# Performance work log

Measured on AMD Instinct MI355X. Metric: run time of the kernel, lower is better.

Reference implementation:

```python
import jax, jax.numpy as jnp
import numpy as np

KERNEL_MUL = 2.0
KERNEL_NUM = 5


def _mmd(source, target):
    n = source.shape[0]
    m = target.shape[0]
    total = jnp.concatenate([source, target], axis=0)  # [n+m, d]
    sq = jnp.sum(total * total, axis=1)  # [n+m]
    l2 = sq[:, None] + sq[None, :] - 2.0 * (total @ total.T)  # [n+m, n+m]
    l2 = jnp.maximum(l2, 0.0)
    n_samples = n + m
    bandwidth = jnp.sum(l2) / (n_samples * n_samples - n_samples)
    bandwidth = bandwidth / (KERNEL_MUL ** (KERNEL_NUM // 2))
    # sum of KERNEL_NUM Gaussian kernels with geometric bandwidths
    kernels = sum(jnp.exp(-l2 / (bandwidth * KERNEL_MUL ** i)) for i in range(KERNEL_NUM))
    b = n  # batch_size = n, as in the torch code
    xx = jnp.sum(kernels[:b, :b]) / (n * n)
    yy = jnp.sum(kernels[b:, b:]) / (m * m)
    xy = jnp.sum(kernels[:b, b:]) / (n * m)
    yx = jnp.sum(kernels[b:, :b]) / (m * n)
    return xx + yy - xy - yx


def setup_inputs() -> dict:
    key = jax.random.key(0)
    k1, k2 = jax.random.split(key)
    source = jax.random.normal(k1, (4096, 256), dtype=jnp.float32)
    target = jax.random.normal(k2, (4096, 256), dtype=jnp.float32)
    return {"source": source, "target": target}


def reference(source, target):
    return _mmd(source, target)
```

## Files before the change

### kernel.cpp

```cpp
#include <hip/hip_runtime.h>
#include <hip/hip_bf16.h>

#define WS_SLOT_OFF   0
#define WS_NEGG_OFF   16640
#define WS_SQPART_OFF 16648
#define WS_CSPART_OFF 17672
#define WS_SQ_OFF     148744
#define WS_G_OFF      181520

#define NROW 8192
#define HALF 4096
#define DIM  256
#define TILE 128
#define NB   64
#define NBLK (NB * (NB + 1) / 2)
#define KC   32
#define NC   (DIM / KC)
#define BUFE (TILE * KC)
#define PREPB 128

typedef short  short8 __attribute__((ext_vector_type(8)));
typedef float  f32x4  __attribute__((ext_vector_type(4)));
typedef float  f32x2  __attribute__((ext_vector_type(2)));
typedef unsigned short us4 __attribute__((ext_vector_type(4)));

static __device__ __forceinline__ unsigned short f2bfbits(float f) {
    __hip_bfloat16 h = __float2bfloat16(f);
    return *reinterpret_cast<unsigned short*>(&h);
}
static __device__ __forceinline__ float bfbits2f(unsigned short u) {
    return __uint_as_float(((unsigned int)u) << 16);
}
static __device__ __forceinline__ void gl_lds16(const void* g, void* l) {
    __builtin_amdgcn_global_load_lds(
        (const __attribute__((address_space(1))) void*)g,
        (__attribute__((address_space(3))) void*)l, 16, 0, 0);
}

__global__ __launch_bounds__(256) void k_prep(const float* __restrict__ src,
                                              const float* __restrict__ tgt,
                                              unsigned short* __restrict__ G,
                                              float* __restrict__ sq,
                                              float* __restrict__ cspart,
                                              double* __restrict__ sqpart) {
    __shared__ float cs_lds[4 * 256];
    __shared__ double sq_lds[4];

    int t = threadIdx.x, wid = t >> 6, lane = t & 63;
    int r0 = blockIdx.x * 64;
    int c4 = lane * 4;

    float cs0 = 0.f, cs1 = 0.f, cs2 = 0.f, cs3 = 0.f;
    double wsq = 0.0;
    for (int i = 0; i < 16; ++i) {
        int row = r0 + wid + i * 4;
        const float* base = (row < HALF) ? (src + (size_t)row * DIM)
                                         : (tgt + (size_t)(row - HALF) * DIM);
        float4 v = *(const float4*)(base + c4);
        unsigned short u0 = f2bfbits(v.x), u1 = f2bfbits(v.y),
                       u2 = f2bfbits(v.z), u3 = f2bfbits(v.w);
        us4 uu = {u0, u1, u2, u3};
        *(us4*)(G + (size_t)row * DIM + c4) = uu;
        float r0f = bfbits2f(u0), r1f = bfbits2f(u1),
              r2f = bfbits2f(u2), r3f = bfbits2f(u3);
        cs0 += r0f; cs1 += r1f; cs2 += r2f; cs3 += r3f;
        float s = r0f * r0f + r1f * r1f + r2f * r2f + r3f * r3f;
        #pragma unroll
        for (int off = 32; off; off >>= 1) s += __shfl_down(s, off);
        if (lane == 0) { sq[row] = s; wsq += (double)s; }
    }
    cs_lds[wid * 256 + c4 + 0] = cs0;
    cs_lds[wid * 256 + c4 + 1] = cs1;
    cs_lds[wid * 256 + c4 + 2] = cs2;
    cs_lds[wid * 256 + c4 + 3] = cs3;
    if (lane == 0) sq_lds[wid] = wsq;
    __syncthreads();
    float s = cs_lds[t] + cs_lds[256 + t] + cs_lds[512 + t] + cs_lds[768 + t];
    cspart[blockIdx.x * 256 + t] = s;
    if (t == 0)
        sqpart[blockIdx.x] = sq_lds[0] + sq_lds[1] + sq_lds[2] + sq_lds[3];
}

__global__ __launch_bounds__(256) void k_bw(const float* __restrict__ cspart,
                                            const double* __restrict__ sqpart,
                                            double* __restrict__ negg) {
    __shared__ double red[256];
    __shared__ double red2[256];
    int t = threadIdx.x;
    double c = 0.0;
    for (int b = 0; b < PREPB; ++b) c += (double)cspart[b * 256 + t];
    double s = (t < PREPB) ? sqpart[t] : 0.0;
    red[t]  = s;
    red2[t] = c * c;
    __syncthreads();
    for (int off = 128; off; off >>= 1) {
        if (t < off) { red[t] += red[t + off]; red2[t] += red2[t + off]; }
        __syncthreads();
    }
    if (t == 0) {
        const double N = (double)NROW;
        double sum_l2 = 2.0 * N * red[0] - 2.0 * red2[0];
        double bw = sum_l2 / (N * N - N);
        bw = bw / 4.0;
        negg[0] = -1.4426950408889634 / (16.0 * bw);
    }
}

__global__ __launch_bounds__(256, 3) void k_mmd(const unsigned short* __restrict__ G,
                                                const float* __restrict__ sq,
                                                const double* __restrict__ negg,
                                                double* __restrict__ slots) {
    __shared__ unsigned short As[2 * BUFE];
    __shared__ unsigned short Bs[2 * BUFE];
    __shared__ double wsum[4];

    int bi = 0, rem = blockIdx.x;
    while (rem >= NB - bi) { rem -= NB - bi; ++bi; }
    int bj = bi + rem;

    int t = threadIdx.x, wid = t >> 6, lane = t & 63;
    int wr = wid >> 1, wc = wid & 1;
    int rl = lane & 15, klane = lane >> 4;

    const unsigned short* Abase = G + (size_t)bi * TILE * DIM;
    const unsigned short* Bbase = G + (size_t)bj * TILE * DIM;

    int lr0 = wid * 32 + (lane >> 2);
    int slog0 = (lane & 3) ^ ((lr0 >> 1) & 3);
    int lr1 = lr0 + 16;
    int slog1 = (lane & 3) ^ ((lr1 >> 1) & 3);
    size_t ga0 = (size_t)lr0 * DIM + slog0 * 8;
    size_t ga1 = (size_t)lr1 * DIM + slog1 * 8;
    int ld0 = (wid * 32) * KC;
    int ld1 = (wid * 32 + 16) * KC;

    int aoff[4], boff[4];
    #pragma unroll
    for (int f = 0; f < 4; ++f) {
        int ra = wr * 64 + f * 16 + rl;
        aoff[f] = ra * KC + ((klane ^ ((ra >> 1) & 3)) * 8);
        int rb = wc * 64 + f * 16 + rl;
        boff[f] = rb * KC + ((klane ^ ((rb >> 1) & 3)) * 8);
    }

    const f32x4 zero4 = {0.f, 0.f, 0.f, 0.f};
    f32x4 acc[4][4];
    #pragma unroll
    for (int i = 0; i < 4; ++i)
        #pragma unroll
        for (int j = 0; j < 4; ++j) acc[i][j] = zero4;

    #define STAGE(kc, b)                                                     \
        do {                                                                 \
            gl_lds16(Abase + ga0 + (kc) * KC, &As[(b) * BUFE + ld0]);        \
            gl_lds16(Bbase + ga0 + (kc) * KC, &Bs[(b) * BUFE + ld0]);        \
            gl_lds16(Abase + ga1 + (kc) * KC, &As[(b) * BUFE + ld1]);        \
            gl_lds16(Bbase + ga1 + (kc) * KC, &Bs[(b) * BUFE + ld1]);        \
        } while (0)

    STAGE(0, 0);
    #pragma unroll
    for (int kc = 0; kc < NC; ++kc) {
        asm volatile("s_waitcnt vmcnt(0)" ::: "memory");
        __builtin_amdgcn_s_barrier();
        __builtin_amdgcn_sched_barrier(0);
        if (kc + 1 < NC) STAGE(kc + 1, (kc + 1) & 1);

        const unsigned short* Ab = &As[(kc & 1) * BUFE];
        const unsigned short* Bb = &Bs[(kc & 1) * BUFE];
        short8 af[4], bfv[4];
        #pragma unroll
        for (int f = 0; f < 4; ++f) {
            af[f]  = *(const short8*)&Ab[aoff[f]];
            bfv[f] = *(const short8*)&Bb[boff[f]];
        }
        #pragma unroll
        for (int i = 0; i < 4; ++i)
            #pragma unroll
            for (int j = 0; j < 4; ++j)
                acc[i][j] = __builtin_amdgcn_mfma_f32_16x16x32_bf16(
                    af[i], bfv[j], acc[i][j], 0, 0, 0);
    }
    #undef STAGE

    int gi0 = bi * TILE + wr * 64;
    int gj0 = bj * TILE + wc * 64;
    float ng2 = (float)negg[0];
    float m2g = -2.0f * ng2;
    f32x2 m2g2 = {m2g, m2g};
    int rgrp = lane >> 4;

    float sqb4[4];
    #pragma unroll
    for (int j = 0; j < 4; ++j) sqb4[j] = sq[gj0 + j * 16 + rl] * ng2;

    f32x2 tsv = {0.f, 0.f};
    #pragma unroll
    for (int i = 0; i < 4; ++i) {
        int base = gi0 + i * 16 + rgrp * 4;
        f32x2 sa01 = {sq[base + 0] * ng2, sq[base + 1] * ng2};
        f32x2 sa23 = {sq[base + 2] * ng2, sq[base + 3] * ng2};
        #pragma unroll
        for (int j = 0; j < 4; ++j) {
            f32x2 sb = {sqb4[j], sqb4[j]};
            f32x2 x01 = {acc[i][j][0], acc[i][j][1]};
            f32x2 x23 = {acc[i][j][2], acc[i][j][3]};
            x01 = x01 * m2g2 + (sa01 + sb);
            x23 = x23 * m2g2 + (sa23 + sb);
            f32x2 e01, e23;
            e01.x = exp2f(x01.x); e01.y = exp2f(x01.y);
            e23.x = exp2f(x23.x); e23.y = exp2f(x23.y);
            f32x2 p01 = e01 * e01, q01 = p01 * p01,
                  r01 = q01 * q01, s01 = r01 * r01;
            f32x2 p23 = e23 * e23, q23 = p23 * p23,
                  r23 = q23 * q23, s23 = r23 * r23;
            tsv += ((e01 + p01) + (q01 + r01)) + s01;
            tsv += ((e23 + p23) + (q23 + r23)) + s23;
        }
    }
    float tsum = tsv.x + tsv.y;

    float w = ((bi < 32) == (bj < 32)) ? 1.f : -1.f;
    if (bi != bj) w *= 2.f;
    double dsum = (double)tsum * (double)w;

    #pragma unroll
    for (int off = 32; off; off >>= 1) dsum += __shfl_down(dsum, off);
    if (lane == 0) wsum[wid] = dsum;
    __syncthreads();
    if (t == 0)
        slots[blockIdx.x] = wsum[0] + wsum[1] + wsum[2] + wsum[3];
}

__global__ __launch_bounds__(256) void k_final(const double* __restrict__ slots,
                                               float* __restrict__ out) {
    __shared__ double red[256];
    int t = threadIdx.x;
    double s = 0.0;
    for (int i = t; i < NBLK; i += 256) s += slots[i];
    red[t] = s;
    __syncthreads();
    for (int off = 128; off; off >>= 1) {
        if (t < off) red[t] += red[t + off];
        __syncthreads();
    }
    if (t == 0)
        out[0] = (float)(red[0] / ((double)HALF * (double)HALF));
}

extern "C" void kernel_launch(void* const* d_in, const int* in_sizes, int n_in,
                              void* d_out, int out_size, void* d_ws, size_t ws_size,
                              hipStream_t stream) {
    const float* src = (const float*)d_in[0];
    const float* tgt = (const float*)d_in[1];
    float* out = (float*)d_out;

    double* slots     = (double*)((char*)d_ws + WS_SLOT_OFF);
    double* negg      = (double*)((char*)d_ws + WS_NEGG_OFF);
    double* sqpart    = (double*)((char*)d_ws + WS_SQPART_OFF);
    float*  cspart    = (float*)((char*)d_ws + WS_CSPART_OFF);
    float*  sq        = (float*)((char*)d_ws + WS_SQ_OFF);
    unsigned short* G = (unsigned short*)((char*)d_ws + WS_G_OFF);

    k_prep<<<PREPB, 256, 0, stream>>>(src, tgt, G, sq, cspart, sqpart);
    k_bw<<<1, 256, 0, stream>>>(cspart, sqpart, negg);
    k_mmd<<<NBLK, 256, 0, stream>>>(G, sq, negg, slots);
    k_final<<<1, 256, 0, stream>>>(slots, out);
}
```

Measured before the change: 65.65 us.

## Shrink MMD tiles to 64x64 with 32x32x16 MFMA and interleaved block order

Measured after the change: 83.12 us. 1.27x slower.

```diff
diff --git a/kernel.cpp b/kernel.cpp
--- a/kernel.cpp
+++ b/kernel.cpp
@@ -2,26 +2,25 @@
 #include <hip/hip_bf16.h>
 
 #define WS_SLOT_OFF   0
-#define WS_NEGG_OFF   16640
-#define WS_SQPART_OFF 16648
-#define WS_CSPART_OFF 17672
-#define WS_SQ_OFF     148744
-#define WS_G_OFF      181520
+#define WS_NEGG_OFF   66048
+#define WS_SQPART_OFF 66056
+#define WS_CSPART_OFF 67080
+#define WS_SQ_OFF     198152
+#define WS_G_OFF      230928
 
 #define NROW 8192
 #define HALF 4096
 #define DIM  256
-#define TILE 128
-#define NB   64
-#define NBLK (NB * (NB + 1) / 2)
+#define TT   64
+#define NT   128
+#define NPAIR (NT * (NT + 1) / 2)
 #define KC   32
 #define NC   (DIM / KC)
-#define BUFE (TILE * KC)
+#define BUFE (TT * KC)
 #define PREPB 128
 
 typedef short  short8 __attribute__((ext_vector_type(8)));
-typedef float  f32x4  __attribute__((ext_vector_type(4)));
-typedef float  f32x2  __attribute__((ext_vector_type(2)));
+typedef float  f32x16 __attribute__((ext_vector_type(16)));
 typedef unsigned short us4 __attribute__((ext_vector_type(4)));
 
 static __device__ __forceinline__ unsigned short f2bfbits(float f) {
@@ -106,7 +105,7 @@
     }
 }
 
-__global__ __launch_bounds__(256, 3) void k_mmd(const unsigned short* __restrict__ G,
+__global__ __launch_bounds__(256, 6) void k_mmd(const unsigned short* __restrict__ G,
                                                 const float* __restrict__ sq,
                                                 const double* __restrict__ negg,
                                                 double* __restrict__ slots) {
@@ -114,48 +113,39 @@
     __shared__ unsigned short Bs[2 * BUFE];
     __shared__ double wsum[4];
 
-    int bi = 0, rem = blockIdx.x;
-    while (rem >= NB - bi) { rem -= NB - bi; ++bi; }
-    int bj = bi + rem;
+    int bid = blockIdx.x;
+    int p = (bid & 7) * (NPAIR / 8) + (bid >> 3);
+
+    int ti = 0, rem = p;
+    while (rem >= NT - ti) { rem -= NT - ti; ++ti; }
+    int tj = ti + rem;
 
     int t = threadIdx.x, wid = t >> 6, lane = t & 63;
     int wr = wid >> 1, wc = wid & 1;
-    int rl = lane & 15, klane = lane >> 4;
-
-    const unsigned short* Abase = G + (size_t)bi * TILE * DIM;
-    const unsigned short* Bbase = G + (size_t)bj * TILE * DIM;
-
-    int lr0 = wid * 32 + (lane >> 2);
-    int slog0 = (lane & 3) ^ ((lr0 >> 1) & 3);
-    int lr1 = lr0 + 16;
-    int slog1 = (lane & 3) ^ ((lr1 >> 1) & 3);
-    size_t ga0 = (size_t)lr0 * DIM + slog0 * 8;
-    size_t ga1 = (size_t)lr1 * DIM + slog1 * 8;
-    int ld0 = (wid * 32) * KC;
-    int ld1 = (wid * 32 + 16) * KC;
-
-    int aoff[4], boff[4];
-    #pragma unroll
-    for (int f = 0; f < 4; ++f) {
-        int ra = wr * 64 + f * 16 + rl;
-        aoff[f] = ra * KC + ((klane ^ ((ra >> 1) & 3)) * 8);
-        int rb = wc * 64 + f * 16 + rl;
-        boff[f] = rb * KC + ((klane ^ ((rb >> 1) & 3)) * 8);
-    }
-
-    const f32x4 zero4 = {0.f, 0.f, 0.f, 0.f};
-    f32x4 acc[4][4];
-    #pragma unroll
-    for (int i = 0; i < 4; ++i)
-        #pragma unroll
-        for (int j = 0; j < 4; ++j) acc[i][j] = zero4;
-
-    #define STAGE(kc, b)                                                     \
-        do {                                                                 \
-            gl_lds16(Abase + ga0 + (kc) * KC, &As[(b) * BUFE + ld0]);        \
-            gl_lds16(Bbase + ga0 + (kc) * KC, &Bs[(b) * BUFE + ld0]);        \
-            gl_lds16(Abase + ga1 + (kc) * KC, &As[(b) * BUFE + ld1]);        \
-            gl_lds16(Bbase + ga1 + (kc) * KC, &Bs[(b) * BUFE + ld1]);        \
+
+    const unsigned short* Abase = G + (size_t)ti * TT * DIM;
+    const unsigned short* Bbase = G + (size_t)tj * TT * DIM;
+
+    int sslot = (lane & 3) ^ ((lane >> 3) & 3);
+    size_t gsrc = (size_t)(wid * 16 + (lane >> 2)) * DIM + sslot * 8;
+    int ldst = (wid * 16) * KC;
+
+    int ra = wr * 32 + (lane & 31);
+    int rb = wc * 32 + (lane & 31);
+    int sA = lane >> 5;
+    int swa = (ra >> 1) & 3, swb = (rb >> 1) & 3;
+    int aoff0 = ra * KC + ((sA ^ swa) * 8);
+    int aoff1 = ra * KC + (((2 + sA) ^ swa) * 8);
+    int boff0 = rb * KC + ((sA ^ swb) * 8);
+    int boff1 = rb * KC + (((2 + sA) ^ swb) * 8);
+
+    f32x16 acc = {0.f, 0.f, 0.f, 0.f, 0.f, 0.f, 0.f, 0.f,
+                  0.f, 0.f, 0.f, 0.f, 0.f, 0.f, 0.f, 0.f};
+
+    #define STAGE(kc, b)                                                   \
+        do {                                                               \
+            gl_lds16(Abase + gsrc + (kc) * KC, &As[(b) * BUFE + ldst]);    \
+            gl_lds16(Bbase + gsrc + (kc) * KC, &Bs[(b) * BUFE + ldst]);    \
         } while (0)
 
     STAGE(0, 0);
@@ -168,68 +158,45 @@
 
         const unsigned short* Ab = &As[(kc & 1) * BUFE];
         const unsigned short* Bb = &Bs[(kc & 1) * BUFE];
-        short8 af[4], bfv[4];
-        #pragma unroll
-        for (int f = 0; f < 4; ++f) {
-            af[f]  = *(const short8*)&Ab[aoff[f]];
-            bfv[f] = *(const short8*)&Bb[boff[f]];
-        }
-        #pragma unroll
-        for (int i = 0; i < 4; ++i)
-            #pragma unroll
-            for (int j = 0; j < 4; ++j)
-                acc[i][j] = __builtin_amdgcn_mfma_f32_16x16x32_bf16(
-                    af[i], bfv[j], acc[i][j], 0, 0, 0);
+        short8 a0 = *(const short8*)&Ab[aoff0];
+        short8 b0 = *(const short8*)&Bb[boff0];
+        short8 a1 = *(const short8*)&Ab[aoff1];
+        short8 b1 = *(const short8*)&Bb[boff1];
+        acc = __builtin_amdgcn_mfma_f32_32x32x16_bf16(a0, b0, acc, 0, 0, 0);
+        acc = __builtin_amdgcn_mfma_f32_32x32x16_bf16(a1, b1, acc, 0, 0, 0);
     }
     #undef STAGE
 
-    int gi0 = bi * TILE + wr * 64;
-    int gj0 = bj * TILE + wc * 64;
+    int gi0 = ti * TT + wr * 32 + 4 * (lane >> 5);
+    int gj  = tj * TT + wc * 32 + (lane & 31);
     float ng2 = (float)negg[0];
     float m2g = -2.0f * ng2;
-    f32x2 m2g2 = {m2g, m2g};
-    int rgrp = lane >> 4;
-
-    float sqb4[4];
+    float sqb = sq[gj] * ng2;
+
+    float tsum = 0.f;
     #pragma unroll
-    for (int j = 0; j < 4; ++j) sqb4[j] = sq[gj0 + j * 16 + rl] * ng2;
-
-    f32x2 tsv = {0.f, 0.f};
-    #pragma unroll
-    for (int i = 0; i < 4; ++i) {
-        int base = gi0 + i * 16 + rgrp * 4;
-        f32x2 sa01 = {sq[base + 0] * ng2, sq[base + 1] * ng2};
-        f32x2 sa23 = {sq[base + 2] * ng2, sq[base + 3] * ng2};
-        #pragma unroll
-        for (int j = 0; j < 4; ++j) {
-            f32x2 sb = {sqb4[j], sqb4[j]};
-            f32x2 x01 = {acc[i][j][0], acc[i][j][1]};
-            f32x2 x23 = {acc[i][j][2], acc[i][j][3]};
-            x01 = x01 * m2g2 + (sa01 + sb);
-            x23 = x23 * m2g2 + (sa23 + sb);
-            f32x2 e01, e23;
-            e01.x = exp2f(x01.x); e01.y = exp2f(x01.y);
-            e23.x = exp2f(x23.x); e23.y = exp2f(x23.y);
-            f32x2 p01 = e01 * e01, q01 = p01 * p01,
-                  r01 = q01 * q01, s01 = r01 * r01;
-            f32x2 p23 = e23 * e23, q23 = p23 * p23,
-                  r23 = q23 * q23, s23 = r23 * r23;
-            tsv += ((e01 + p01) + (q01 + r01)) + s01;
-            tsv += ((e23 + p23) + (q23 + r23)) + s23;
-        }
-    }
-    float tsum = tsv.x + tsv.y;
-
-    float w = ((bi < 32) == (bj < 32)) ? 1.f : -1.f;
-    if (bi != bj) w *= 2.f;
-    double dsum = (double)tsum * (double)w;
+    for (int q = 0; q < 16; ++q) {
+        int row = (q & 3) + 8 * (q >> 2);
+        float sqa = sq[gi0 + row] * ng2;
+        float x   = fmaf(acc[q], m2g, sqa + sqb);
+        float e   = exp2f(x);
+        float e2  = e * e;
+        float e4  = e2 * e2;
+        float e8  = e4 * e4;
+        float e16 = e8 * e8;
+        tsum += (e + e2) + (e4 + e8) + e16;
+    }
+
+    float w = ((ti < NT / 2) == (tj < NT / 2)) ? 1.f : -1.f;
+    if (ti != tj) w *= 2.f;
+    double dsum = (double)(tsum * w);
 
     #pragma unroll
     for (int off = 32; off; off >>= 1) dsum += __shfl_down(dsum, off);
     if (lane == 0) wsum[wid] = dsum;
     __syncthreads();
     if (t == 0)
-        slots[blockIdx.x] = wsum[0] + wsum[1] + wsum[2] + wsum[3];
+        slots[bid] = wsum[0] + wsum[1] + wsum[2] + wsum[3];
 }
 
 __global__ __launch_bounds__(256) void k_final(const double* __restrict__ slots,
@@ -237,7 +204,7 @@
     __shared__ double red[256];
     int t = threadIdx.x;
     double s = 0.0;
-    for (int i = t; i < NBLK; i += 256) s += slots[i];
+    for (int i = t; i < NPAIR; i += 256) s += slots[i];
     red[t] = s;
     __syncthreads();
     for (int off = 128; off; off >>= 1) {
@@ -264,6 +231,6 @@
 
     k_prep<<<PREPB, 256, 0, stream>>>(src, tgt, G, sq, cspart, sqpart);
     k_bw<<<1, 256, 0, stream>>>(cspart, sqpart, negg);
-    k_mmd<<<NBLK, 256, 0, stream>>>(G, sq, negg, slots);
+    k_mmd<<<NPAIR, 256, 0, stream>>>(G, sq, negg, slots);
     k_final<<<1, 256, 0, stream>>>(slots, out);
 }
```

## Use 256x256 tiles with 512-thread blocks each processing three tile pairs

Applied to the files above, without the earlier changes.

Measured after the change: 70.16 us. +6.9%, slower.

```diff
diff --git a/kernel.cpp b/kernel.cpp
--- a/kernel.cpp
+++ b/kernel.cpp
@@ -2,22 +2,23 @@
 #include <hip/hip_bf16.h>
 
 #define WS_SLOT_OFF   0
-#define WS_NEGG_OFF   16640
-#define WS_SQPART_OFF 16648
-#define WS_CSPART_OFF 17672
-#define WS_SQ_OFF     148744
-#define WS_G_OFF      181520
+#define WS_NEGG_OFF   1408
+#define WS_SQPART_OFF 1416
+#define WS_CSPART_OFF 3464
+#define WS_SQ_OFF     265608
+#define WS_G_OFF      298384
 
 #define NROW 8192
 #define HALF 4096
 #define DIM  256
-#define TILE 128
-#define NB   64
-#define NBLK (NB * (NB + 1) / 2)
+#define TS   256
+#define NTT  32
+#define NP   (NTT * (NTT + 1) / 2)
+#define GRID_MMD (NP / 3)
 #define KC   32
 #define NC   (DIM / KC)
-#define BUFE (TILE * KC)
-#define PREPB 128
+#define ABUF (TS * KC)
+#define PREPB 256
 
 typedef short  short8 __attribute__((ext_vector_type(8)));
 typedef float  f32x4  __attribute__((ext_vector_type(4)));
@@ -47,12 +48,12 @@
     __shared__ double sq_lds[4];
 
     int t = threadIdx.x, wid = t >> 6, lane = t & 63;
-    int r0 = blockIdx.x * 64;
+    int r0 = blockIdx.x * 32;
     int c4 = lane * 4;
 
     float cs0 = 0.f, cs1 = 0.f, cs2 = 0.f, cs3 = 0.f;
     double wsq = 0.0;
-    for (int i = 0; i < 16; ++i) {
+    for (int i = 0; i < 8; ++i) {
         int row = r0 + wid + i * 4;
         const float* base = (row < HALF) ? (src + (size_t)row * DIM)
                                          : (tgt + (size_t)(row - HALF) * DIM);
@@ -89,7 +90,7 @@
     int t = threadIdx.x;
     double c = 0.0;
     for (int b = 0; b < PREPB; ++b) c += (double)cspart[b * 256 + t];
-    double s = (t < PREPB) ? sqpart[t] : 0.0;
+    double s = sqpart[t];
     red[t]  = s;
     red2[t] = c * c;
     __syncthreads();
@@ -106,139 +107,148 @@
     }
 }
 
-__global__ __launch_bounds__(256, 3) void k_mmd(const unsigned short* __restrict__ G,
+__global__ __launch_bounds__(512, 2) void k_mmd(const unsigned short* __restrict__ G,
                                                 const float* __restrict__ sq,
                                                 const double* __restrict__ negg,
                                                 double* __restrict__ slots) {
-    __shared__ unsigned short As[2 * BUFE];
-    __shared__ unsigned short Bs[2 * BUFE];
-    __shared__ double wsum[4];
-
-    int bi = 0, rem = blockIdx.x;
-    while (rem >= NB - bi) { rem -= NB - bi; ++bi; }
-    int bj = bi + rem;
-
+    __shared__ unsigned short As[2 * ABUF];
+    __shared__ unsigned short Bs[2 * ABUF];
+    __shared__ double wsum[8];
+
+    int bid = blockIdx.x;
     int t = threadIdx.x, wid = t >> 6, lane = t & 63;
-    int wr = wid >> 1, wc = wid & 1;
+    int wr = wid >> 2, wc = wid & 3;
     int rl = lane & 15, klane = lane >> 4;
 
-    const unsigned short* Abase = G + (size_t)bi * TILE * DIM;
-    const unsigned short* Bbase = G + (size_t)bj * TILE * DIM;
-
-    int lr0 = wid * 32 + (lane >> 2);
-    int slog0 = (lane & 3) ^ ((lr0 >> 1) & 3);
-    int lr1 = lr0 + 16;
-    int slog1 = (lane & 3) ^ ((lr1 >> 1) & 3);
-    size_t ga0 = (size_t)lr0 * DIM + slog0 * 8;
-    size_t ga1 = (size_t)lr1 * DIM + slog1 * 8;
-    int ld0 = (wid * 32) * KC;
-    int ld1 = (wid * 32 + 16) * KC;
-
-    int aoff[4], boff[4];
+    int slog = (lane & 3) ^ ((lane >> 3) & 3);
+    size_t gs = (size_t)(wid * 32 + (lane >> 2)) * DIM + slog * 8;
+    int ldst = (wid * 32) * KC;
+
+    int aoff[8], boff[4];
     #pragma unroll
-    for (int f = 0; f < 4; ++f) {
-        int ra = wr * 64 + f * 16 + rl;
+    for (int f = 0; f < 8; ++f) {
+        int ra = wr * 128 + f * 16 + rl;
         aoff[f] = ra * KC + ((klane ^ ((ra >> 1) & 3)) * 8);
-        int rb = wc * 64 + f * 16 + rl;
-        boff[f] = rb * KC + ((klane ^ ((rb >> 1) & 3)) * 8);
-    }
-
-    const f32x4 zero4 = {0.f, 0.f, 0.f, 0.f};
-    f32x4 acc[4][4];
+    }
     #pragma unroll
-    for (int i = 0; i < 4; ++i)
-        #pragma unroll
-        for (int j = 0; j < 4; ++j) acc[i][j] = zero4;
-
-    #define STAGE(kc, b)                                                     \
-        do {                                                                 \
-            gl_lds16(Abase + ga0 + (kc) * KC, &As[(b) * BUFE + ld0]);        \
-            gl_lds16(Bbase + ga0 + (kc) * KC, &Bs[(b) * BUFE + ld0]);        \
-            gl_lds16(Abase + ga1 + (kc) * KC, &As[(b) * BUFE + ld1]);        \
-            gl_lds16(Bbase + ga1 + (kc) * KC, &Bs[(b) * BUFE + ld1]);        \
-        } while (0)
-
-    STAGE(0, 0);
-    #pragma unroll
-    for (int kc = 0; kc < NC; ++kc) {
-        asm volatile("s_waitcnt vmcnt(0)" ::: "memory");
-        __builtin_amdgcn_s_barrier();
-        __builtin_amdgcn_sched_barrier(0);
-        if (kc + 1 < NC) STAGE(kc + 1, (kc + 1) & 1);
-
-        const unsigned short* Ab = &As[(kc & 1) * BUFE];
-        const unsigned short* Bb = &Bs[(kc & 1) * BUFE];
-        short8 af[4], bfv[4];
-        #pragma unroll
-        for (int f = 0; f < 4; ++f) {
-            af[f]  = *(const short8*)&Ab[aoff[f]];
-            bfv[f] = *(const short8*)&Bb[boff[f]];
-        }
-        #pragma unroll
-        for (int i = 0; i < 4; ++i)
-            #pragma unroll
-            for (int j = 0; j < 4; ++j)
-                acc[i][j] = __builtin_amdgcn_mfma_f32_16x16x32_bf16(
-                    af[i], bfv[j], acc[i][j], 0, 0, 0);
-    }
-    #undef STAGE
-
-    int gi0 = bi * TILE + wr * 64;
-    int gj0 = bj * TILE + wc * 64;
+    for (int g = 0; g < 4; ++g) {
+        int rb = wc * 64 + g * 16 + rl;
+        boff[g] = rb * KC + ((klane ^ ((rb >> 1) & 3)) * 8);
+    }
+
     float ng2 = (float)negg[0];
     float m2g = -2.0f * ng2;
     f32x2 m2g2 = {m2g, m2g};
-    int rgrp = lane >> 4;
-
-    float sqb4[4];
+
+    double bsum = 0.0;
+
+    #define STAGE(kc, b)                                                       \
+        do {                                                                   \
+            gl_lds16(Abase + gs + (kc) * KC,                                   \
+                     &As[(b) * ABUF + ldst]);                                  \
+            gl_lds16(Abase + gs + (size_t)16 * DIM + (kc) * KC,                \
+                     &As[(b) * ABUF + ldst + 16 * KC]);                        \
+            gl_lds16(Bbase + gs + (kc) * KC,                                   \
+                     &Bs[(b) * ABUF + ldst]);                                  \
+            gl_lds16(Bbase + gs + (size_t)16 * DIM + (kc) * KC,                \
+                     &Bs[(b) * ABUF + ldst + 16 * KC]);                        \
+        } while (0)
+
+    for (int pi = 0; pi < 3; ++pi) {
+        int p = bid * 3 + pi;
+        int ti = 0, rem = p;
+        while (rem >= NTT - ti) { rem -= NTT - ti; ++ti; }
+        int tj = ti + rem;
+
+        const unsigned short* Abase = G + (size_t)ti * TS * DIM;
+        const unsigned short* Bbase = G + (size_t)tj * TS * DIM;
+
+        const f32x4 zero4 = {0.f, 0.f, 0.f, 0.f};
+        f32x4 acc[8][4];
+        #pragma unroll
+        for (int f = 0; f < 8; ++f)
+            #pragma unroll
+            for (int g = 0; g < 4; ++g) acc[f][g] = zero4;
+
+        STAGE(0, 0);
+        #pragma unroll
+        for (int kc = 0; kc < NC; ++kc) {
+            asm volatile("s_waitcnt vmcnt(0)" ::: "memory");
+            __builtin_amdgcn_s_barrier();
+            __builtin_amdgcn_sched_barrier(0);
+            if (kc + 1 < NC) STAGE(kc + 1, (kc + 1) & 1);
+
+            const unsigned short* Ab = &As[(kc & 1) * ABUF];
+            const unsigned short* Bb = &Bs[(kc & 1) * ABUF];
+            short8 af[8], bfv[4];
+            #pragma unroll
+            for (int f = 0; f < 8; ++f) af[f]  = *(const short8*)&Ab[aoff[f]];
+            #pragma unroll
+            for (int g = 0; g < 4; ++g) bfv[g] = *(const short8*)&Bb[boff[g]];
+            #pragma unroll
+            for (int f = 0; f < 8; ++f)
+                #pragma unroll
+                for (int g = 0; g < 4; ++g)
+                    acc[f][g] = __builtin_amdgcn_mfma_f32_16x16x32_bf16(
+                        af[f], bfv[g], acc[f][g], 0, 0, 0);
+        }
+
+        int gi0 = ti * TS + wr * 128;
+        int gj0 = tj * TS + wc * 64;
+
+        float sqb4[4];
+        #pragma unroll
+        for (int g = 0; g < 4; ++g) sqb4[g] = sq[gj0 + g * 16 + rl] * ng2;
+
+        f32x2 tsv = {0.f, 0.f};
+        #pragma unroll
+        for (int f = 0; f < 8; ++f) {
+            int base = gi0 + f * 16 + klane * 4;
+            f32x2 sa01 = {sq[base + 0] * ng2, sq[base + 1] * ng2};
+            f32x2 sa23 = {sq[base + 2] * ng2, sq[base + 3] * ng2};
+            #pragma unroll
+            for (int g = 0; g < 4; ++g) {
+                f32x2 sb = {sqb4[g], sqb4[g]};
+                f32x2 x01 = {acc[f][g][0], acc[f][g][1]};
+                f32x2 x23 = {acc[f][g][2], acc[f][g][3]};
+                x01 = x01 * m2g2 + (sa01 + sb);
+                x23 = x23 * m2g2 + (sa23 + sb);
+                f32x2 e01, e23;
+                e01.x = exp2f(x01.x); e01.y = exp2f(x01.y);
+                e23.x = exp2f(x23.x); e23.y = exp2f(x23.y);
+                f32x2 p01 = e01 * e01, q01 = p01 * p01,
+                      r01 = q01 * q01, s01 = r01 * r01;
+                f32x2 p23 = e23 * e23, q23 = p23 * p23,
+                      r23 = q23 * q23, s23 = r23 * r23;
+                tsv += ((e01 + p01) + (q01 + r01)) + s01;
+                tsv += ((e23 + p23) + (q23 + r23)) + s23;
+            }
+        }
+        float tsum = tsv.x + tsv.y;
+
+        float w = ((ti < NTT / 2) == (tj < NTT / 2)) ? 1.f : -1.f;
+        if (ti != tj) w *= 2.f;
+        bsum += (double)(tsum * w);
+    }
+    #undef STAGE
+
     #pragma unroll
-    for (int j = 0; j < 4; ++j) sqb4[j] = sq[gj0 + j * 16 + rl] * ng2;
-
-    f32x2 tsv = {0.f, 0.f};
-    #pragma unroll
-    for (int i = 0; i < 4; ++i) {
-        int base = gi0 + i * 16 + rgrp * 4;
-        f32x2 sa01 = {sq[base + 0] * ng2, sq[base + 1] * ng2};
-        f32x2 sa23 = {sq[base + 2] * ng2, sq[base + 3] * ng2};
-        #pragma unroll
-        for (int j = 0; j < 4; ++j) {
-            f32x2 sb = {sqb4[j], sqb4[j]};
-            f32x2 x01 = {acc[i][j][0], acc[i][j][1]};
-            f32x2 x23 = {acc[i][j][2], acc[i][j][3]};
-            x01 = x01 * m2g2 + (sa01 + sb);
-            x23 = x23 * m2g2 + (sa23 + sb);
-            f32x2 e01, e23;
-            e01.x = exp2f(x01.x); e01.y = exp2f(x01.y);
-            e23.x = exp2f(x23.x); e23.y = exp2f(x23.y);
-            f32x2 p01 = e01 * e01, q01 = p01 * p01,
-                  r01 = q01 * q01, s01 = r01 * r01;
-            f32x2 p23 = e23 * e23, q23 = p23 * p23,
-                  r23 = q23 * q23, s23 = r23 * r23;
-            tsv += ((e01 + p01) + (q01 + r01)) + s01;
-            tsv += ((e23 + p23) + (q23 + r23)) + s23;
-        }
-    }
-    float tsum = tsv.x + tsv.y;
-
-    float w = ((bi < 32) == (bj < 32)) ? 1.f : -1.f;
-    if (bi != bj) w *= 2.f;
-    double dsum = (double)tsum * (double)w;
-
-    #pragma unroll
-    for (int off = 32; off; off >>= 1) dsum += __shfl_down(dsum, off);
-    if (lane == 0) wsum[wid] = dsum;
-    __syncthreads();
-    if (t == 0)
-        slots[blockIdx.x] = wsum[0] + wsum[1] + wsum[2] + wsum[3];
+    for (int off = 32; off; off >>= 1) bsum += __shfl_down(bsum, off);
+    if (lane == 0) wsum[wid] = bsum;
+    __syncthreads();
+    if (t == 0) {
+        double s = 0.0;
+        #pragma unroll
+        for (int i = 0; i < 8; ++i) s += wsum[i];
+        slots[bid] = s;
+    }
 }
 
 __global__ __launch_bounds__(256) void k_final(const double* __restrict__ slots,
                                                float* __restrict__ out) {
     __shared__ double red[256];
     int t = threadIdx.x;
-    double s = 0.0;
-    for (int i = t; i < NBLK; i += 256) s += slots[i];
-    red[t] = s;
+    red[t] = (t < GRID_MMD) ? slots[t] : 0.0;
     __syncthreads();
     for (int off = 128; off; off >>= 1) {
         if (t < off) red[t] += red[t + off];
@@ -264,6 +274,6 @@
 
     k_prep<<<PREPB, 256, 0, stream>>>(src, tgt, G, sq, cspart, sqpart);
     k_bw<<<1, 256, 0, stream>>>(cspart, sqpart, negg);
-    k_mmd<<<NBLK, 256, 0, stream>>>(G, sq, negg, slots);
+    k_mmd<<<GRID_MMD, 512, 0, stream>>>(G, sq, negg, slots);
     k_final<<<1, 256, 0, stream>>>(slots, out);
 }
```
